# Kernel tuning notes

Hardware: AMD Instinct MI355X
Metric: run time of the kernel (lower is better)

The kernel has to match this reference:

```python
import jax, jax.numpy as jnp
import numpy as np

B, C, D, H = 1024, 119, 1024, 16
DH = D // H  # head dim = 64
EPS = 1e-5


def setup_inputs() -> dict:
    key = jax.random.key(0)
    ks = jax.random.split(key, 16)
    s = lambda n: 1.0 / np.sqrt(n)
    return {
        "board_tensor": jax.random.normal(ks[0], (B, C, 8, 8), jnp.float32),
        "emb_W": jax.random.normal(ks[1], (C, D), jnp.float32) * s(C),
        "emb_b": jnp.zeros((D,), jnp.float32),
        "positional": jnp.zeros((1, 64, D), jnp.float32),
        "Wq": jax.random.normal(ks[2], (D, D), jnp.float32) * s(D),
        "bq": jnp.zeros((D,), jnp.float32),
        "Wk": jax.random.normal(ks[3], (D, D), jnp.float32) * s(D),
        "bk": jnp.zeros((D,), jnp.float32),
        "Wv": jax.random.normal(ks[4], (D, D), jnp.float32) * s(D),
        "bv": jnp.zeros((D,), jnp.float32),
        "Wo": jax.random.normal(ks[5], (D, D), jnp.float32) * s(D),
        "bo": jnp.zeros((D,), jnp.float32),
        "rel_bias": jax.random.normal(ks[6], (H, 64, 64), jnp.float32) * 0.02,
        "ln_g": jnp.ones((D,), jnp.float32),
        "ln_b": jnp.zeros((D,), jnp.float32),
    }


def _layernorm(x, g, b):
    mu = jnp.mean(x, axis=-1, keepdims=True)
    var = jnp.mean(jnp.square(x - mu), axis=-1, keepdims=True)
    return (x - mu) * jax.lax.rsqrt(var + EPS) * g + b


def reference(board_tensor, emb_W, emb_b, positional, Wq, bq, Wk, bk, Wv, bv,
              Wo, bo, rel_bias, ln_g, ln_b):
    b = board_tensor.shape[0]
    # (B, C, 8, 8) -> (B, 64, C)
    x = board_tensor.reshape(b, C, 64).transpose(0, 2, 1)
    x = x @ emb_W + emb_b            # embedding GEMM -> (B, 64, D)
    x = x + positional
    # chess relative attention with learned per-head 64x64 bias
    q = (x @ Wq + bq).reshape(b, 64, H, DH)
    k = (x @ Wk + bk).reshape(b, 64, H, DH)
    v = (x @ Wv + bv).reshape(b, 64, H, DH)
    scores = jnp.einsum('bqhd,bkhd->bhqk', q, k) / np.sqrt(DH) + rel_bias
    attn = jax.nn.softmax(scores, axis=-1)
    o = jnp.einsum('bhqk,bkhd->bqhd', attn, v).reshape(b, 64, D)
    o = o @ Wo + bo
    # residual + LayerNorm
    return _layernorm(x + o, ln_g, ln_b)
```

## Files before the change

### kernel.cpp

```cpp
#include <hip/hip_runtime.h>
#include <hip/hip_bf16.h>
#include <stdint.h>


typedef float  floatx4 __attribute__((ext_vector_type(4)));
typedef short  bf16x8  __attribute__((ext_vector_type(8)));
typedef short  bf16x4  __attribute__((ext_vector_type(4)));

__device__ __forceinline__ short f2bf(float f) {
  __hip_bfloat16 h = __float2bfloat16(f);
  return *reinterpret_cast<short*>(&h);
}
__device__ __forceinline__ float bf2f(short s) {
  union { float f; uint32_t u; } c;
  c.u = ((uint32_t)(uint16_t)s) << 16;
  return c.f;
}
__device__ __forceinline__ floatx4 mfma16(bf16x8 a, bf16x8 b, floatx4 c) {
  return __builtin_amdgcn_mfma_f32_16x16x32_bf16(a, b, c, 0, 0, 0);
}

#define ASYNC_CP16(gsrc, ldst)                                                 \
  __builtin_amdgcn_global_load_lds(                                            \
      (const __attribute__((address_space(1))) void*)(gsrc),                   \
      (__attribute__((address_space(3))) void*)(ldst), 16, 0, 0)

__global__ void k_transpose_bf16(const float* __restrict__ src,
                                 short* __restrict__ dst) {
  __shared__ float tile[32][33];
  const int bx = blockIdx.x * 32, by = blockIdx.y * 32;
  const int tx = threadIdx.x, ty = threadIdx.y;
#pragma unroll
  for (int i = 0; i < 32; i += 8)
    tile[ty + i][tx] = src[(size_t)(by + ty + i) * 1024 + bx + tx];
  __syncthreads();
#pragma unroll
  for (int i = 0; i < 32; i += 8)
    dst[(size_t)(bx + ty + i) * 1024 + by + tx] = f2bf(tile[tx][ty + i]);
}

__global__ void k_embWt(const float* __restrict__ embW, short* __restrict__ dst) {
  const int idx = blockIdx.x * 256 + threadIdx.x;
  const int n = idx >> 7, c = idx & 127;
  dst[idx] = f2bf((c < 119) ? embW[(size_t)c * 1024 + n] : 0.f);
}

__global__ __launch_bounds__(256) void k_embed(
    const float* __restrict__ board, const short* __restrict__ embWt,
    const float* __restrict__ emb_b, const float* __restrict__ pos,
    short* __restrict__ x) {
  __shared__ short As[64 * 136];
  __shared__ short Bs[128 * 32];
  const int t = threadIdx.x, l = t & 63, w = t >> 6;
  const int quad = l >> 4, lan = l & 15;
  const int xcd = blockIdx.x & 7;
  const int lin = (blockIdx.x >> 3) + xcd * 1024;
  const int b = lin >> 3, nBase = (lin & 7) << 7;
  const float* bb = board + (size_t)b * (119 * 64);
  const int s = t & 63;
#pragma unroll
  for (int it = 0; it < 16; ++it) {
    const int c0 = ((t >> 6) + it * 4) * 2;
    float u0 = (c0 < 119) ? bb[c0 * 64 + s] : 0.f;
    float u1 = (c0 + 1 < 119) ? bb[(c0 + 1) * 64 + s] : 0.f;
    short2 pr; pr.x = f2bf(u0); pr.y = f2bf(u1);
    *(short2*)&As[s * 136 + c0] = pr;
  }
  const short* Bg0 = embWt + (size_t)(nBase + (t >> 2)) * 128 + (t & 3) * 8;
  const short* Bg1 = Bg0 + (size_t)64 * 128;
  short* Bs0 = &Bs[(w * 16) * 32];
  short* Bs1 = &Bs[(64 + w * 16) * 32];
  floatx4 acc[4][2] = {};
  __syncthreads();
  for (int kk = 0; kk < 4; ++kk) {
    ASYNC_CP16(Bg0 + kk * 32, Bs0);
    ASYNC_CP16(Bg1 + kk * 32, Bs1);
    __syncthreads();
    bf16x8 af[4], bfr[2];
#pragma unroll
    for (int mt = 0; mt < 4; ++mt)
      af[mt] = *(const bf16x8*)&As[(mt * 16 + lan) * 136 + kk * 32 + quad * 8];
#pragma unroll
    for (int n2 = 0; n2 < 2; ++n2)
      bfr[n2] = *(const bf16x8*)&Bs[(w * 32 + n2 * 16 + lan) * 32 + quad * 8];
#pragma unroll
    for (int mt = 0; mt < 4; ++mt)
#pragma unroll
      for (int n2 = 0; n2 < 2; ++n2)
        acc[mt][n2] = mfma16(af[mt], bfr[n2], acc[mt][n2]);
    __syncthreads();
  }
#pragma unroll
  for (int n2 = 0; n2 < 2; ++n2) {
    const int n = nBase + w * 32 + n2 * 16 + lan;
    const float bi = emb_b[n];
#pragma unroll
    for (int mt = 0; mt < 4; ++mt) {
      const int s0 = mt * 16 + quad * 4;
      floatx4 v = acc[mt][n2];
#pragma unroll
      for (int r = 0; r < 4; ++r) {
        const int ss = s0 + r;
        x[((size_t)b * 64 + ss) * 1024 + n] = f2bf(v[r] + bi + pos[ss * 1024 + n]);
      }
    }
  }
}

__device__ __forceinline__ void gemm8_core(
    const short* __restrict__ A, const short* __restrict__ Bt,
    short* lds, const int mBase, const int nBase, floatx4 (&acc)[8][4]) {
  const int t = threadIdx.x;
  const int w = t >> 6, l = t & 63;
  const int lan = l & 15, quad = l >> 4;
  const int wm = w >> 2, wn = w & 3;
  const int row0 = t >> 2;
  const int sg = (t & 3) ^ ((t >> 3) & 3);
  const short* Ag = A + (size_t)(mBase + row0) * 1024 + sg * 8;
  const short* Bg = Bt + (size_t)(nBase + row0) * 1024 + sg * 8;
  const int swz = (quad ^ ((lan >> 1) & 3)) * 8;
  const int aRd = (wm * 128 + lan) * 32 + swz;
  const int bRd = 32768 + (wn * 64 + lan) * 32 + swz;
  const int wst = w * 512;

#define STAGE_A8(ktgt, kh, buf) do {                                          \
    const short* _s = Ag + (ktgt) * 64 + (kh) * 32;                           \
    ASYNC_CP16(_s,          &lds[(buf) * 16384 + (kh) * 8192 + wst]);          \
    ASYNC_CP16(_s + 131072, &lds[(buf) * 16384 + (kh) * 8192 + 4096 + wst]);   \
  } while (0)
#define STAGE_B8(ktgt, kh, buf) do {                                          \
    const short* _s = Bg + (ktgt) * 64 + (kh) * 32;                           \
    ASYNC_CP16(_s,          &lds[32768 + (buf) * 16384 + (kh) * 8192 + wst]);  \
    ASYNC_CP16(_s + 131072,                                                    \
               &lds[32768 + (buf) * 16384 + (kh) * 8192 + 4096 + wst]);        \
  } while (0)
#define LDA8(dst, buf, ks, mh)                                                \
    _Pragma("unroll") for (int mf = 0; mf < 4; ++mf)                          \
      dst[mf] = *(const bf16x8*)&lds[(buf) * 16384 + (ks) * 8192 + aRd +      \
                                     ((mh) * 64 + mf * 16) * 32];
#define LDB8(dst, buf, ks)                                                    \
    _Pragma("unroll") for (int nf = 0; nf < 4; ++nf)                          \
      dst[nf] = *(const bf16x8*)&lds[(buf) * 16384 + (ks) * 8192 + bRd +      \
                                     nf * 512];
#define MMA8(mh, bfr)                                                         \
    _Pragma("unroll") for (int mf = 0; mf < 4; ++mf)                          \
      _Pragma("unroll") for (int nf = 0; nf < 4; ++nf)                        \
        acc[(mh) * 4 + mf][nf] = mfma16(af[mf], bfr[nf], acc[(mh) * 4 + mf][nf]);
#define PHASE_MID                                                             \
    __builtin_amdgcn_sched_barrier(0);                                        \
    __builtin_amdgcn_s_barrier();                                             \
    asm volatile("s_waitcnt lgkmcnt(0)" ::: "memory");                        \
    __builtin_amdgcn_sched_barrier(0);                                        \
    __builtin_amdgcn_s_setprio(1)
#define PHASE_END                                                             \
    __builtin_amdgcn_s_setprio(0);                                            \
    __builtin_amdgcn_sched_barrier(0);                                        \
    __builtin_amdgcn_s_barrier()

  STAGE_A8(0, 0, 0); STAGE_B8(0, 0, 0);
  STAGE_A8(0, 1, 0); STAGE_B8(0, 1, 0);
  STAGE_A8(1, 0, 1); STAGE_B8(1, 0, 1);
  asm volatile("s_waitcnt vmcnt(4)" ::: "memory");
  __builtin_amdgcn_sched_barrier(0);
  __builtin_amdgcn_s_barrier();

#define TILE8(kt, cur) do {                                                   \
    const int k1 = ((kt) + 1 < 16) ? (kt) + 1 : 15;                           \
    const int k2 = ((kt) + 2 < 16) ? (kt) + 2 : 15;                           \
    bf16x8 af[4], bf0[4], bf1[4];                                             \
                                                          \
    LDA8(af, cur, 0, 0); LDB8(bf0, cur, 0);                                   \
    STAGE_A8(k1, 1, (cur) ^ 1);                                               \
    PHASE_MID; MMA8(0, bf0); PHASE_END;                                       \
                                                          \
    LDA8(af, cur, 0, 1);                                                      \
    STAGE_B8(k1, 1, (cur) ^ 1);                                               \
    PHASE_MID; MMA8(1, bf0); PHASE_END;                                       \
                                                          \
    LDA8(af, cur, 1, 0); LDB8(bf1, cur, 1);                                   \
    STAGE_A8(k2, 0, cur);                                                     \
    PHASE_MID; MMA8(0, bf1); PHASE_END;                                       \
                                                          \
    LDA8(af, cur, 1, 1);                                                      \
    STAGE_B8(k2, 0, cur);                                                     \
    asm volatile("s_waitcnt vmcnt(4)" ::: "memory");                          \
    PHASE_MID; MMA8(1, bf1); PHASE_END;                                       \
  } while (0)

#pragma unroll 1
  for (int it = 0; it < 8; ++it) {
    TILE8(it * 2, 0);
    TILE8(it * 2 + 1, 1);
  }
  asm volatile("s_waitcnt vmcnt(0)" ::: "memory");
#undef TILE8
#undef PHASE_END
#undef PHASE_MID
#undef MMA8
#undef LDB8
#undef LDA8
#undef STAGE_B8
#undef STAGE_A8
}

__global__ __launch_bounds__(512, 2) void k_gemm_qkv8(
    const short* __restrict__ A, const short* __restrict__ Bt,
    const float* __restrict__ bq, const float* __restrict__ bk,
    const float* __restrict__ bv, short* __restrict__ qb,
    short* __restrict__ kb, short* __restrict__ vtb) {
  __shared__ short lds[65536];
  const int xcd = blockIdx.x & 7;
  const int lin = (blockIdx.x >> 3) + xcd * 384;
  const int grp = lin / 96;
  const int rem = lin - grp * 96;
  const int mBase = ((grp << 3) + (rem & 7)) << 8;
  const int nBase = (rem >> 3) << 8;

  floatx4 acc[8][4] = {};
  gemm8_core(A, Bt, lds, mBase, nBase, acc);

  const int t = threadIdx.x, w = t >> 6, l = t & 63;
  const int lan = l & 15, quad = l >> 4;
  const int wm = w >> 2, wn = w & 3;
  const int region = nBase >> 10;
  const int nb = nBase & 1023;
  const float* bias = (region == 0) ? bq : (region == 1) ? bk : bv;
  short* qk = (region == 0) ? qb : kb;
#pragma unroll
  for (int am = 0; am < 8; ++am) {
    const int m0 = mBase + wm * 128 + am * 16 + quad * 4;
    const int b = m0 >> 6, s0 = m0 & 63;
#pragma unroll
    for (int nf = 0; nf < 4; ++nf) {
      const int nn = nb + wn * 64 + nf * 16 + lan;
      const int h = nn >> 6, dh = nn & 63;
      const float bi = bias[nn];
      floatx4 v = acc[am][nf];
      if (region < 2) {
        short* dst = qk + (((size_t)b * 16 + h) * 64 + s0) * 64 + dh;
        dst[0]   = f2bf(v.x + bi);
        dst[64]  = f2bf(v.y + bi);
        dst[128] = f2bf(v.z + bi);
        dst[192] = f2bf(v.w + bi);
      } else {
        bf16x4 pk = {f2bf(v.x + bi), f2bf(v.y + bi), f2bf(v.z + bi), f2bf(v.w + bi)};
        *(bf16x4*)(vtb + (((size_t)b * 16 + h) * 64 + dh) * 64 + s0) = pk;
      }
    }
  }
}

__global__ __launch_bounds__(512, 2) void k_gemm_oproj8(
    const short* __restrict__ A, const short* __restrict__ Bt,
    const float* __restrict__ bo, const short* __restrict__ xres,
    short* __restrict__ y) {
  __shared__ short lds[65536];
  const int xcd = blockIdx.x & 7;
  const int lin = (blockIdx.x >> 3) + xcd * 128;
  const int grp = lin >> 5;
  const int rem = lin & 31;
  const int mBase = ((grp << 3) + (rem & 7)) << 8;
  const int nBase = (rem >> 3) << 8;

  floatx4 acc[8][4] = {};
  gemm8_core(A, Bt, lds, mBase, nBase, acc);

  const int t = threadIdx.x, w = t >> 6, l = t & 63;
  const int lan = l & 15, quad = l >> 4;
  const int wm = w >> 2, wn = w & 3;
#pragma unroll
  for (int nf = 0; nf < 4; ++nf) {
    const int n = nBase + wn * 64 + nf * 16 + lan;
    const float bi = bo[n];
#pragma unroll
    for (int am = 0; am < 8; ++am) {
      const int m0 = mBase + wm * 128 + am * 16 + quad * 4;
      floatx4 v = acc[am][nf];
#pragma unroll
      for (int r = 0; r < 4; ++r) {
        const size_t idx = (size_t)(m0 + r) * 1024 + n;
        y[idx] = f2bf(v[r] + bi + bf2f(xres[idx]));
      }
    }
  }
}

__global__ __launch_bounds__(256) void k_attn(
    const short* __restrict__ qb, const short* __restrict__ kb,
    const short* __restrict__ vtb, const float* __restrict__ rel_bias,
    short* __restrict__ ob) {
  __shared__ short P[4][64 * 72];
  const int t = threadIdx.x, l = t & 63, w = t >> 6;
  const int quad = l >> 4, lan = l & 15;
  const int b = blockIdx.x >> 2;
  const int h = (blockIdx.x & 3) * 4 + w;
  const short* q  = qb  + ((size_t)b * 16 + h) * 4096;
  const short* kp = kb  + ((size_t)b * 16 + h) * 4096;
  const short* vt = vtb + ((size_t)b * 16 + h) * 4096;
  const float* bias = rel_bias + (size_t)h * 4096;
  short* Pw = &P[w][0];

  bf16x8 kf[4][2], qf[4][2];
#pragma unroll
  for (int mt = 0; mt < 4; ++mt) {
    kf[mt][0] = *(const bf16x8*)&kp[(mt * 16 + lan) * 64 + quad * 8];
    kf[mt][1] = *(const bf16x8*)&kp[(mt * 16 + lan) * 64 + 32 + quad * 8];
  }
#pragma unroll
  for (int nt = 0; nt < 4; ++nt) {
    qf[nt][0] = *(const bf16x8*)&q[(nt * 16 + lan) * 64 + quad * 8];
    qf[nt][1] = *(const bf16x8*)&q[(nt * 16 + lan) * 64 + 32 + quad * 8];
  }
  floatx4 S[4][4];
#pragma unroll
  for (int mt = 0; mt < 4; ++mt)
#pragma unroll
    for (int nt = 0; nt < 4; ++nt) {
      floatx4 z = {0.f, 0.f, 0.f, 0.f};
      z = mfma16(kf[mt][0], qf[nt][0], z);
      S[mt][nt] = mfma16(kf[mt][1], qf[nt][1], z);
    }
  float rs[4];
#pragma unroll
  for (int nt = 0; nt < 4; ++nt) {
    const int qi = nt * 16 + lan;
    float sv[4][4];
    float m = -1e30f;
#pragma unroll
    for (int mt = 0; mt < 4; ++mt) {
      floatx4 bi = *(const floatx4*)&bias[qi * 64 + mt * 16 + quad * 4];
#pragma unroll
      for (int r = 0; r < 4; ++r) {
        sv[mt][r] = fmaf(S[mt][nt][r], 0.125f, bi[r]);
        m = fmaxf(m, sv[mt][r]);
      }
    }
    m = fmaxf(m, __shfl_xor(m, 16));
    m = fmaxf(m, __shfl_xor(m, 32));
    float sum = 0.f;
#pragma unroll
    for (int mt = 0; mt < 4; ++mt) {
      float p0 = exp2f((sv[mt][0] - m) * 1.4426950408889634f);
      float p1 = exp2f((sv[mt][1] - m) * 1.4426950408889634f);
      float p2 = exp2f((sv[mt][2] - m) * 1.4426950408889634f);
      float p3 = exp2f((sv[mt][3] - m) * 1.4426950408889634f);
      sum += p0 + p1 + p2 + p3;
      bf16x4 pk = {f2bf(p0), f2bf(p1), f2bf(p2), f2bf(p3)};
      *(bf16x4*)&Pw[qi * 72 + mt * 16 + quad * 4] = pk;
    }
    sum += __shfl_xor(sum, 16);
    sum += __shfl_xor(sum, 32);
    rs[nt] = 1.0f / sum;
  }
  bf16x8 pf[4][2];
#pragma unroll
  for (int nt = 0; nt < 4; ++nt) {
    pf[nt][0] = *(const bf16x8*)&Pw[(nt * 16 + lan) * 72 + quad * 8];
    pf[nt][1] = *(const bf16x8*)&Pw[(nt * 16 + lan) * 72 + 32 + quad * 8];
  }
#pragma unroll
  for (int mo = 0; mo < 4; ++mo) {
    bf16x8 vf0 = *(const bf16x8*)&vt[(mo * 16 + lan) * 64 + quad * 8];
    bf16x8 vf1 = *(const bf16x8*)&vt[(mo * 16 + lan) * 64 + 32 + quad * 8];
#pragma unroll
    for (int nt = 0; nt < 4; ++nt) {
      floatx4 z = {0.f, 0.f, 0.f, 0.f};
      z = mfma16(vf0, pf[nt][0], z);
      z = mfma16(vf1, pf[nt][1], z);
      const int qi = nt * 16 + lan;
      const int dh0 = mo * 16 + quad * 4;
      const float r = rs[nt];
      bf16x4 pk = {f2bf(z.x * r), f2bf(z.y * r), f2bf(z.z * r), f2bf(z.w * r)};
      *(bf16x4*)&ob[((size_t)b * 64 + qi) * 1024 + h * 64 + dh0] = pk;
    }
  }
}

__global__ __launch_bounds__(256) void k_ln(
    const short* __restrict__ y, const float* __restrict__ g,
    const float* __restrict__ be, float* __restrict__ out) {
  const int row = blockIdx.x;
  const int t = threadIdx.x;
  const short* yr = y + (size_t)row * 1024;
  bf16x4 v4 = *(const bf16x4*)&yr[t * 4];
  float v0 = bf2f(v4.x), v1 = bf2f(v4.y), v2 = bf2f(v4.z), v3 = bf2f(v4.w);
  float s = v0 + v1 + v2 + v3;
  float s2 = v0 * v0 + v1 * v1 + v2 * v2 + v3 * v3;
#pragma unroll
  for (int off = 1; off < 64; off <<= 1) {
    s  += __shfl_xor(s, off);
    s2 += __shfl_xor(s2, off);
  }
  __shared__ float red[8];
  const int w = t >> 6;
  if ((t & 63) == 0) { red[w] = s; red[w + 4] = s2; }
  __syncthreads();
  s  = red[0] + red[1] + red[2] + red[3];
  s2 = red[4] + red[5] + red[6] + red[7];
  const float mu = s * (1.f / 1024.f);
  const float var = s2 * (1.f / 1024.f) - mu * mu;
  const float rstd = rsqrtf(var + 1e-5f);
  const int c = t * 4;
  float4 o;
  o.x = (v0 - mu) * rstd * g[c]     + be[c];
  o.y = (v1 - mu) * rstd * g[c + 1] + be[c + 1];
  o.z = (v2 - mu) * rstd * g[c + 2] + be[c + 2];
  o.w = (v3 - mu) * rstd * g[c + 3] + be[c + 3];
  *(float4*)&out[(size_t)row * 1024 + c] = o;
}

extern "C" void kernel_launch(void* const* d_in, const int* in_sizes, int n_in,
                              void* d_out, int out_size, void* d_ws,
                              size_t ws_size, hipStream_t stream) {
  const float* board    = (const float*)d_in[0];
  const float* emb_W    = (const float*)d_in[1];
  const float* emb_b    = (const float*)d_in[2];
  const float* pos      = (const float*)d_in[3];
  const float* Wq       = (const float*)d_in[4];
  const float* bq       = (const float*)d_in[5];
  const float* Wk       = (const float*)d_in[6];
  const float* bk       = (const float*)d_in[7];
  const float* Wv       = (const float*)d_in[8];
  const float* bv       = (const float*)d_in[9];
  const float* Wo       = (const float*)d_in[10];
  const float* bo       = (const float*)d_in[11];
  const float* rel_bias = (const float*)d_in[12];
  const float* ln_g     = (const float*)d_in[13];
  const float* ln_b     = (const float*)d_in[14];

  char* ws = (char*)d_ws;
  short* Wqkv_t = (short*)ws; ws += (size_t)3072 * 1024 * 2;
  short* Wo_t   = (short*)ws; ws += (size_t)1024 * 1024 * 2;
  short* embWt  = (short*)ws; ws += (size_t)1024 * 128 * 2;
  short* xb     = (short*)ws; ws += (size_t)65536 * 1024 * 2;
  short* qb     = (short*)ws; ws += (size_t)16384 * 4096 * 2;
  short* kb     = (short*)ws; ws += (size_t)16384 * 4096 * 2;
  short* vtb    = (short*)ws; ws += (size_t)16384 * 4096 * 2;
  short* ob     = (short*)ws; ws += (size_t)65536 * 1024 * 2;
  short* yb     = kb;

  dim3 tb(32, 8);
  k_transpose_bf16<<<dim3(32, 32), tb, 0, stream>>>(Wq, Wqkv_t);
  k_transpose_bf16<<<dim3(32, 32), tb, 0, stream>>>(Wk, Wqkv_t + (size_t)1024 * 1024);
  k_transpose_bf16<<<dim3(32, 32), tb, 0, stream>>>(Wv, Wqkv_t + (size_t)2 * 1024 * 1024);
  k_transpose_bf16<<<dim3(32, 32), tb, 0, stream>>>(Wo, Wo_t);
  k_embWt<<<512, 256, 0, stream>>>(emb_W, embWt);

  k_embed<<<8192, 256, 0, stream>>>(board, embWt, emb_b, pos, xb);
  k_gemm_qkv8<<<3072, 512, 0, stream>>>(xb, Wqkv_t, bq, bk, bv, qb, kb, vtb);
  k_attn<<<4096, 256, 0, stream>>>(qb, kb, vtb, rel_bias, ob);
  k_gemm_oproj8<<<1024, 512, 0, stream>>>(ob, Wo_t, bo, xb, yb);
  k_ln<<<65536, 256, 0, stream>>>(yb, ln_g, ln_b, (float*)d_out);
}
```

Measured before the change: 1.359 ms.

## Shrink GEMM tiles to 128x128 with smaller LDS and higher occupancy

Replaces the 256x256-tile GEMM core used by the QKV and output-projection kernels with a 128x128-tile core. Each wave now holds 2x4 accumulators instead of 8x4, and the block uses half the LDS. Launch bounds go from 2 to 4 blocks per CU, with four times as many blocks. The aim is to improve occupancy and latency hiding, at the cost of lower data reuse per tile, more global and LDS traffic per FLOP, and more barriers per unit of work.

```diff
diff --git a/kernel.cpp b/kernel.cpp
--- a/kernel.cpp
+++ b/kernel.cpp
@@ -107,134 +107,107 @@
   }
 }
 
-__device__ __forceinline__ void gemm8_core(
+__device__ __forceinline__ void gemm128_core(
     const short* __restrict__ A, const short* __restrict__ Bt,
-    short* lds, const int mBase, const int nBase, floatx4 (&acc)[8][4]) {
+    short* lds, const int mBase, const int nBase, floatx4 (&acc)[2][4]) {
   const int t = threadIdx.x;
   const int w = t >> 6, l = t & 63;
   const int lan = l & 15, quad = l >> 4;
-  const int wm = w >> 2, wn = w & 3;
-  const int row0 = t >> 2;
-  const int sg = (t & 3) ^ ((t >> 3) & 3);
-  const short* Ag = A + (size_t)(mBase + row0) * 1024 + sg * 8;
-  const short* Bg = Bt + (size_t)(nBase + row0) * 1024 + sg * 8;
-  const int swz = (quad ^ ((lan >> 1) & 3)) * 8;
-  const int aRd = (wm * 128 + lan) * 32 + swz;
-  const int bRd = 32768 + (wn * 64 + lan) * 32 + swz;
+  const int wm = w >> 1, wn = w & 1;
+  const int srow = t >> 2;
+  const int sg = ((t & 3) ^ ((t >> 2) & 3)) * 8;
+  const short* Ag = A + (size_t)(mBase + srow) * 1024 + sg;
+  const short* Bg = Bt + (size_t)(nBase + srow) * 1024 + sg;
+  const int swz = (quad ^ (lan & 3)) * 8;
+  const int aRd = (wm * 32 + lan) * 32 + swz;
+  const int bRd = 8192 + (wn * 64 + lan) * 32 + swz;
   const int wst = w * 512;
 
-#define STAGE_A8(ktgt, kh, buf) do {                                          \
-    const short* _s = Ag + (ktgt) * 64 + (kh) * 32;                           \
-    ASYNC_CP16(_s,          &lds[(buf) * 16384 + (kh) * 8192 + wst]);          \
-    ASYNC_CP16(_s + 131072, &lds[(buf) * 16384 + (kh) * 8192 + 4096 + wst]);   \
+#define STAGE_AB(ko, kh, buf) do {                                            \
+    ASYNC_CP16(Ag + (ko) + (kh) * 32,                                         \
+               &lds[(buf) * 16384 + (kh) * 4096 + wst]);                       \
+    ASYNC_CP16(Bg + (ko) + (kh) * 32,                                         \
+               &lds[8192 + (buf) * 16384 + (kh) * 4096 + wst]);                \
   } while (0)
-#define STAGE_B8(ktgt, kh, buf) do {                                          \
-    const short* _s = Bg + (ktgt) * 64 + (kh) * 32;                           \
-    ASYNC_CP16(_s,          &lds[32768 + (buf) * 16384 + (kh) * 8192 + wst]);  \
-    ASYNC_CP16(_s + 131072,                                                    \
-               &lds[32768 + (buf) * 16384 + (kh) * 8192 + 4096 + wst]);        \
-  } while (0)
-#define LDA8(dst, buf, ks, mh)                                                \
-    _Pragma("unroll") for (int mf = 0; mf < 4; ++mf)                          \
-      dst[mf] = *(const bf16x8*)&lds[(buf) * 16384 + (ks) * 8192 + aRd +      \
-                                     ((mh) * 64 + mf * 16) * 32];
-#define LDB8(dst, buf, ks)                                                    \
+
+#define PHASE(buf, kh, stko, stkh, stbuf) do {                                \
+    bf16x8 af[2], bfr[4];                                                     \
+    _Pragma("unroll") for (int am = 0; am < 2; ++am)                          \
+      af[am] = *(const bf16x8*)&lds[(buf) * 16384 + (kh) * 4096 + aRd +       \
+                                    am * 512];                                 \
     _Pragma("unroll") for (int nf = 0; nf < 4; ++nf)                          \
-      dst[nf] = *(const bf16x8*)&lds[(buf) * 16384 + (ks) * 8192 + bRd +      \
-                                     nf * 512];
-#define MMA8(mh, bfr)                                                         \
-    _Pragma("unroll") for (int mf = 0; mf < 4; ++mf)                          \
-      _Pragma("unroll") for (int nf = 0; nf < 4; ++nf)                        \
-        acc[(mh) * 4 + mf][nf] = mfma16(af[mf], bfr[nf], acc[(mh) * 4 + mf][nf]);
-#define PHASE_MID                                                             \
+      bfr[nf] = *(const bf16x8*)&lds[(buf) * 16384 + (kh) * 4096 + bRd +      \
+                                     nf * 512];                                \
+    STAGE_AB(stko, stkh, stbuf);                                              \
     __builtin_amdgcn_sched_barrier(0);                                        \
     __builtin_amdgcn_s_barrier();                                             \
     asm volatile("s_waitcnt lgkmcnt(0)" ::: "memory");                        \
     __builtin_amdgcn_sched_barrier(0);                                        \
-    __builtin_amdgcn_s_setprio(1)
-#define PHASE_END                                                             \
+    __builtin_amdgcn_s_setprio(1);                                            \
+    _Pragma("unroll") for (int am = 0; am < 2; ++am)                          \
+      _Pragma("unroll") for (int nf = 0; nf < 4; ++nf)                        \
+        acc[am][nf] = mfma16(af[am], bfr[nf], acc[am][nf]);                   \
     __builtin_amdgcn_s_setprio(0);                                            \
     __builtin_amdgcn_sched_barrier(0);                                        \
-    __builtin_amdgcn_s_barrier()
-
-  STAGE_A8(0, 0, 0); STAGE_B8(0, 0, 0);
-  STAGE_A8(0, 1, 0); STAGE_B8(0, 1, 0);
-  STAGE_A8(1, 0, 1); STAGE_B8(1, 0, 1);
+    asm volatile("s_waitcnt vmcnt(4)" ::: "memory");                          \
+    __builtin_amdgcn_s_barrier();                                             \
+  } while (0)
+
+  STAGE_AB(0, 0, 0);
+  STAGE_AB(0, 1, 0);
+  STAGE_AB(64, 0, 1);
   asm volatile("s_waitcnt vmcnt(4)" ::: "memory");
   __builtin_amdgcn_sched_barrier(0);
   __builtin_amdgcn_s_barrier();
 
-#define TILE8(kt, cur) do {                                                   \
-    const int k1 = ((kt) + 1 < 16) ? (kt) + 1 : 15;                           \
-    const int k2 = ((kt) + 2 < 16) ? (kt) + 2 : 15;                           \
-    bf16x8 af[4], bf0[4], bf1[4];                                             \
-                                                          \
-    LDA8(af, cur, 0, 0); LDB8(bf0, cur, 0);                                   \
-    STAGE_A8(k1, 1, (cur) ^ 1);                                               \
-    PHASE_MID; MMA8(0, bf0); PHASE_END;                                       \
-                                                          \
-    LDA8(af, cur, 0, 1);                                                      \
-    STAGE_B8(k1, 1, (cur) ^ 1);                                               \
-    PHASE_MID; MMA8(1, bf0); PHASE_END;                                       \
-                                                          \
-    LDA8(af, cur, 1, 0); LDB8(bf1, cur, 1);                                   \
-    STAGE_A8(k2, 0, cur);                                                     \
-    PHASE_MID; MMA8(0, bf1); PHASE_END;                                       \
-                                                          \
-    LDA8(af, cur, 1, 1);                                                      \
-    STAGE_B8(k2, 0, cur);                                                     \
-    asm volatile("s_waitcnt vmcnt(4)" ::: "memory");                          \
-    PHASE_MID; MMA8(1, bf1); PHASE_END;                                       \
-  } while (0)
-
 #pragma unroll 1
-  for (int it = 0; it < 8; ++it) {
-    TILE8(it * 2, 0);
-    TILE8(it * 2 + 1, 1);
+  for (int tt = 0; tt < 16; tt += 2) {
+    const int k1 = (tt + 1) * 64;
+    const int k2 = (tt + 2 < 16 ? tt + 2 : 15) * 64;
+    const int k3 = (tt + 3 < 16 ? tt + 3 : 15) * 64;
+    PHASE(0, 0, k1, 1, 1);
+    PHASE(0, 1, k2, 0, 0);
+    PHASE(1, 0, k2, 1, 0);
+    PHASE(1, 1, k3, 0, 1);
   }
   asm volatile("s_waitcnt vmcnt(0)" ::: "memory");
-#undef TILE8
-#undef PHASE_END
-#undef PHASE_MID
-#undef MMA8
-#undef LDB8
-#undef LDA8
-#undef STAGE_B8
-#undef STAGE_A8
-}
-
-__global__ __launch_bounds__(512, 2) void k_gemm_qkv8(
+  __builtin_amdgcn_s_barrier();
+#undef PHASE
+#undef STAGE_AB
+}
+
+__global__ __launch_bounds__(512, 4) void k_gemm_qkv9(
     const short* __restrict__ A, const short* __restrict__ Bt,
     const float* __restrict__ bq, const float* __restrict__ bk,
     const float* __restrict__ bv, short* __restrict__ qb,
     short* __restrict__ kb, short* __restrict__ vtb) {
-  __shared__ short lds[65536];
+  __shared__ short lds[32768];
   const int xcd = blockIdx.x & 7;
-  const int lin = (blockIdx.x >> 3) + xcd * 384;
-  const int grp = lin / 96;
-  const int rem = lin - grp * 96;
-  const int mBase = ((grp << 3) + (rem & 7)) << 8;
-  const int nBase = (rem >> 3) << 8;
-
-  floatx4 acc[8][4] = {};
-  gemm8_core(A, Bt, lds, mBase, nBase, acc);
+  const int lin = (blockIdx.x >> 3) + xcd * 1536;
+  const int grp = lin / 192;
+  const int rem = lin - grp * 192;
+  const int mBase = ((grp << 3) + (rem & 7)) << 7;
+  const int nBase = (rem >> 3) << 7;
+
+  floatx4 acc[2][4] = {};
+  gemm128_core(A, Bt, lds, mBase, nBase, acc);
 
   const int t = threadIdx.x, w = t >> 6, l = t & 63;
   const int lan = l & 15, quad = l >> 4;
-  const int wm = w >> 2, wn = w & 3;
+  const int wm = w >> 1, wn = w & 1;
   const int region = nBase >> 10;
   const int nb = nBase & 1023;
   const float* bias = (region == 0) ? bq : (region == 1) ? bk : bv;
   short* qk = (region == 0) ? qb : kb;
 #pragma unroll
-  for (int am = 0; am < 8; ++am) {
-    const int m0 = mBase + wm * 128 + am * 16 + quad * 4;
-    const int b = m0 >> 6, s0 = m0 & 63;
-#pragma unroll
-    for (int nf = 0; nf < 4; ++nf) {
-      const int nn = nb + wn * 64 + nf * 16 + lan;
-      const int h = nn >> 6, dh = nn & 63;
-      const float bi = bias[nn];
+  for (int nf = 0; nf < 4; ++nf) {
+    const int nn = nb + wn * 64 + nf * 16 + lan;
+    const int h = nn >> 6, dh = nn & 63;
+    const float bi = bias[nn];
+#pragma unroll
+    for (int am = 0; am < 2; ++am) {
+      const int m0 = mBase + wm * 32 + am * 16 + quad * 4;
+      const int b = m0 >> 6, s0 = m0 & 63;
       floatx4 v = acc[am][nf];
       if (region < 2) {
         short* dst = qk + (((size_t)b * 16 + h) * 64 + s0) * 64 + dh;
@@ -250,31 +223,31 @@
   }
 }
 
-__global__ __launch_bounds__(512, 2) void k_gemm_oproj8(
+__global__ __launch_bounds__(512, 4) void k_gemm_oproj9(
     const short* __restrict__ A, const short* __restrict__ Bt,
     const float* __restrict__ bo, const short* __restrict__ xres,
     short* __restrict__ y) {
-  __shared__ short lds[65536];
+  __shared__ short lds[32768];
   const int xcd = blockIdx.x & 7;
-  const int lin = (blockIdx.x >> 3) + xcd * 128;
-  const int grp = lin >> 5;
-  const int rem = lin & 31;
-  const int mBase = ((grp << 3) + (rem & 7)) << 8;
-  const int nBase = (rem >> 3) << 8;
-
-  floatx4 acc[8][4] = {};
-  gemm8_core(A, Bt, lds, mBase, nBase, acc);
+  const int lin = (blockIdx.x >> 3) + xcd * 512;
+  const int grp = lin >> 6;
+  const int rem = lin & 63;
+  const int mBase = ((grp << 3) + (rem & 7)) << 7;
+  const int nBase = (rem >> 3) << 7;
+
+  floatx4 acc[2][4] = {};
+  gemm128_core(A, Bt, lds, mBase, nBase, acc);
 
   const int t = threadIdx.x, w = t >> 6, l = t & 63;
   const int lan = l & 15, quad = l >> 4;
-  const int wm = w >> 2, wn = w & 3;
+  const int wm = w >> 1, wn = w & 1;
 #pragma unroll
   for (int nf = 0; nf < 4; ++nf) {
     const int n = nBase + wn * 64 + nf * 16 + lan;
     const float bi = bo[n];
 #pragma unroll
-    for (int am = 0; am < 8; ++am) {
-      const int m0 = mBase + wm * 128 + am * 16 + quad * 4;
+    for (int am = 0; am < 2; ++am) {
+      const int m0 = mBase + wm * 32 + am * 16 + quad * 4;
       floatx4 v = acc[am][nf];
 #pragma unroll
       for (int r = 0; r < 4; ++r) {
@@ -447,8 +420,8 @@
   k_embWt<<<512, 256, 0, stream>>>(emb_W, embWt);
 
   k_embed<<<8192, 256, 0, stream>>>(board, embWt, emb_b, pos, xb);
-  k_gemm_qkv8<<<3072, 512, 0, stream>>>(xb, Wqkv_t, bq, bk, bv, qb, kb, vtb);
+  k_gemm_qkv9<<<12288, 512, 0, stream>>>(xb, Wqkv_t, bq, bk, bv, qb, kb, vtb);
   k_attn<<<4096, 256, 0, stream>>>(qb, kb, vtb, rel_bias, ob);
-  k_gemm_oproj8<<<1024, 512, 0, stream>>>(ob, Wo_t, bo, xb, yb);
+  k_gemm_oproj9<<<4096, 512, 0, stream>>>(ob, Wo_t, bo, xb, yb);
   k_ln<<<65536, 256, 0, stream>>>(yb, ln_g, ln_b, (float*)d_out);
 }
```

New measurement: 1.315 ms. 3.3% less time.
